# Kernel tuning notes

Hardware: AMD Instinct MI355X
Metric: run time of the kernel (lower is better)

## Reference

```python
import jax, jax.numpy as jnp
import numpy as np

B, S, D = 2, 2048, 1024
H, HD = 16, 64          # num_heads, head_dim
K = 32                  # JL n_components


def setup_inputs() -> dict:
    key = jax.random.key(0)
    k1, k2, k3, k4 = jax.random.split(key, 4)
    return {
        "hidden_states": jax.random.normal(k1, (B, S, D), dtype=jnp.float32),
        "W_attn": jax.random.normal(k2, (D, 3 * D), dtype=jnp.float32) * 0.02,
        "b_attn": jnp.zeros((3 * D,), dtype=jnp.float32),
        "S_proj": jax.random.normal(k3, (K, HD), dtype=jnp.float32) / np.sqrt(K),
        "W_proj": jax.random.normal(k4, (D, D), dtype=jnp.float32) * 0.02,
        "b_proj": jnp.zeros((D,), dtype=jnp.float32),
    }


def reference(hidden_states, W_attn, b_attn, S_proj, W_proj, b_proj):
    b, s, d = hidden_states.shape
    # GPT2 Conv1D: x @ W + b, then split into q,k,v
    qkv = hidden_states @ W_attn + b_attn            # [B,S,3D]
    q, k, v = jnp.split(qkv, 3, axis=-1)
    # split heads -> [B,H,S,HD]
    def split_heads(x):
        return x.reshape(b, s, H, HD).transpose(0, 2, 1, 3)
    q = split_heads(q) @ S_proj.T                    # [B,H,S,K] JL-reduced
    k = split_heads(k) @ S_proj.T                    # [B,H,S,K]
    v = split_heads(v)                               # [B,H,S,HD]
    # naive attention: scale by sqrt(value head_dim) per GPT2 _attn
    scores = jnp.einsum("bhqk,bhsk->bhqs", q, k) / jnp.sqrt(
        jnp.asarray(HD, dtype=v.dtype))              # [B,H,S,S]
    causal = jnp.tril(jnp.ones((s, s), dtype=bool))
    mask_value = jnp.finfo(scores.dtype).min
    scores = jnp.where(causal, scores, mask_value)
    attn = jax.nn.softmax(scores, axis=-1)
    out = jnp.einsum("bhqs,bhsd->bhqd", attn, v)     # [B,H,S,HD]
    out = out.transpose(0, 2, 1, 3).reshape(b, s, d)  # merge heads
    return out @ W_proj + b_proj
```

## Files before the change

kernel.cpp:

```cpp
#include <hip/hip_runtime.h>
#include <hip/hip_bf16.h>
#include <stdint.h>

#define B_ 2
#define S_ 2048
#define D_ 1024
#define H_ 16
#define HD_ 64
#define KJL 32
#define N3 3072
#define N2 2048

typedef __attribute__((ext_vector_type(8))) __bf16 bf16x8;
typedef __attribute__((ext_vector_type(4))) float floatx4;
typedef __attribute__((ext_vector_type(4))) short short4v;
typedef __attribute__((ext_vector_type(2))) unsigned int uint2v;

__device__ __forceinline__ unsigned short f2b(float x) {
  union { float f; unsigned u; } v; v.f = x;
  unsigned r = v.u + 0x7fffu + ((v.u >> 16) & 1u);
  return (unsigned short)(r >> 16);
}

__device__ __forceinline__ unsigned int pkbf(float lo, float hi) {
  union { float f; unsigned u; } a, b;
  a.f = lo; b.f = hi;
  return __builtin_amdgcn_perm(b.u + 0x8000u, a.u + 0x8000u, 0x07060302u);
}

__device__ __forceinline__ void async16(const void* g, void* l) {
  __builtin_amdgcn_global_load_lds((__attribute__((address_space(1))) void*)(g),
                                   (__attribute__((address_space(3))) void*)(l),
                                   16, 0, 0);
}

__global__ __launch_bounds__(256)
void prep_kernel(const float* __restrict__ hidden, unsigned short* __restrict__ hB,
                 const float* __restrict__ W_attn, const float* __restrict__ b_attn,
                 const float* __restrict__ Sp, const float* __restrict__ W_proj,
                 unsigned short* __restrict__ Bt2, unsigned short* __restrict__ WpT,
                 float* __restrict__ bias2) {
  __shared__ float shmem[2048];
  const int bid = blockIdx.x;
  const int tid = threadIdx.x;

  if (bid < 512) {
    const int n4 = (B_ * S_ * D_) / 4;
    int i = bid * 256 + tid;
    for (; i < n4; i += 512 * 256) {
      float4 v = *(const float4*)(hidden + 4 * (size_t)i);
      short4v o = {(short)f2b(v.x), (short)f2b(v.y), (short)f2b(v.z), (short)f2b(v.w)};
      *(short4v*)(hB + 4 * (size_t)i) = o;
    }
  } else if (bid < 2560) {
    const float* in;
    unsigned short* out;
    int Cs, local;
    if (bid < 1536) { local = bid - 512;  in = W_attn + 2048; out = Bt2 + 1024 * 1024; Cs = N3; }
    else            { local = bid - 1536; in = W_proj;        out = WpT;               Cs = D_; }
    float (*t)[33] = (float(*)[33])shmem;
    int c0 = (local & 31) * 32, r0 = (local >> 5) * 32;
    int tx = tid & 31, ty = tid >> 5;
    for (int j = 0; j < 32; j += 8)
      t[ty + j][tx] = in[(size_t)(r0 + ty + j) * Cs + c0 + tx];
    __syncthreads();
    for (int j = 0; j < 32; j += 8)
      out[(size_t)(c0 + ty + j) * D_ + r0 + tx] = f2b(t[tx][ty + j]);
  } else {
    const int lb = bid - 2560;
    const int part = lb >> 6;
    const int h = (lb >> 2) & 15;
    const int dc = lb & 3;
    for (int i = tid; i < 32 * 64; i += 256) shmem[i] = Sp[i];
    __syncthreads();
    const float scale = part ? 1.0f : 0.125f * 1.44269504f;
    const int d = dc * 256 + tid;
    float w[64];
    const float* src = W_attn + (size_t)d * N3 + part * D_ + h * 64;
    for (int j = 0; j < 16; ++j) {
      float4 v = *(const float4*)&src[j * 4];
      w[j * 4 + 0] = v.x; w[j * 4 + 1] = v.y; w[j * 4 + 2] = v.z; w[j * 4 + 3] = v.w;
    }
    const int nbase = part * 512 + h * 32;
    for (int kjl = 0; kjl < 32; ++kjl) {
      float acc = 0.f;
      for (int hd = 0; hd < 64; ++hd) acc += w[hd] * shmem[kjl * 64 + hd];
      Bt2[(size_t)(nbase + kjl) * D_ + d] = f2b(acc * scale);
    }
    if (dc == 0 && tid < 32) {
      float acc = 0.f;
      for (int hd = 0; hd < 64; ++hd) acc += b_attn[part * D_ + h * 64 + hd] * shmem[tid * 64 + hd];
      bias2[nbase + tid] = acc * scale;
    }
  }
}

__global__ __launch_bounds__(256, 2)
void qkv2_gemm_kernel(const unsigned short* __restrict__ A,
                      const unsigned short* __restrict__ Bt,
                      const float* __restrict__ b_attn,
                      const float* __restrict__ bias2,
                      unsigned short* __restrict__ Qjl,
                      unsigned short* __restrict__ Kjl,
                      unsigned short* __restrict__ Vc) {
  __shared__ __align__(16) unsigned short As[2][128 * 32];
  __shared__ __align__(16) unsigned short Bs[2][128 * 32];
  const int tid = threadIdx.x;
  const int lane = tid & 63, wv = tid >> 6;
  const int quad = lane >> 4, col = lane & 15;
  const int wm = wv >> 1, wn = wv & 1;
  const int m0 = blockIdx.y * 128, n0 = blockIdx.x * 128;

  floatx4 acc[4][4] = {};

  for (int kk = 0; kk < D_; kk += 64) {
    for (int it = 0; it < 4; ++it) {
      int c = it * 256 + tid;
      int ks = c >> 9, row = (c >> 2) & 127, kc = c & 3;
      async16(A + (size_t)(m0 + row) * D_ + kk + ks * 32 + kc * 8,
              (unsigned short*)As + c * 8);
    }
    for (int it = 0; it < 4; ++it) {
      int c = it * 256 + tid;
      int ks = c >> 9, row = (c >> 2) & 127, kc = c & 3;
      async16(Bt + (size_t)(n0 + row) * D_ + kk + ks * 32 + kc * 8,
              (unsigned short*)Bs + c * 8);
    }
    asm volatile("s_waitcnt vmcnt(0)" ::: "memory");
    __syncthreads();
    for (int ks = 0; ks < 2; ++ks) {
      bf16x8 af[4], bfr[4];
      for (int mt = 0; mt < 4; ++mt)
        af[mt] = *(const bf16x8*)&As[ks][(wm * 64 + mt * 16 + col) * 32 + quad * 8];
      for (int nt = 0; nt < 4; ++nt)
        bfr[nt] = *(const bf16x8*)&Bs[ks][(wn * 64 + nt * 16 + col) * 32 + quad * 8];
      for (int mt = 0; mt < 4; ++mt)
        for (int nt = 0; nt < 4; ++nt)
          acc[mt][nt] = __builtin_amdgcn_mfma_f32_16x16x32_bf16(
              af[mt], bfr[nt], acc[mt][nt], 0, 0, 0);
    }
    __syncthreads();
  }

  const int pq = n0 >> 9;
  for (int mt = 0; mt < 4; ++mt) {
    int gm0 = m0 + wm * 64 + mt * 16 + quad * 4;
    int b = gm0 >> 11, s = gm0 & (S_ - 1);
    for (int nt = 0; nt < 4; ++nt) {
      int gn = n0 + wn * 64 + nt * 16 + col;
      if (pq >= 2) {
        int vcol = gn - 1024;
        float bs = b_attn[2048 + vcol];
        int h = vcol >> 6, hd = vcol & 63;
        short4v vv;
        for (int i = 0; i < 4; ++i)
          vv[i] = (short)f2b(acc[mt][nt][i] + bs);
        size_t idx = ((((size_t)(b * H_ + h) * 64 + (s >> 5)) * 64 + hd) * 32 + (s & 31));
        *(short4v*)&Vc[idx] = vv;
      } else {
        float bs = bias2[gn];
        int gl = gn & 511;
        int h = gl >> 5, kjl = gl & 31;
        unsigned short* dst = pq ? Kjl : Qjl;
        size_t base = ((size_t)(b * H_ + h) * S_ + s) * KJL + kjl;
        for (int i = 0; i < 4; ++i)
          dst[base + (size_t)i * KJL] = f2b(acc[mt][nt][i] + bs);
      }
    }
  }
}

__global__ __launch_bounds__(256, 2)
void attn_kernel(const unsigned short* __restrict__ Qjl,
                 const unsigned short* __restrict__ Kjl,
                 const unsigned short* __restrict__ Vc,
                 unsigned short* __restrict__ AO) {
  __shared__ __align__(16) unsigned short Ps[4][32 * 136];
  const int tid = threadIdx.x;
  const int lane = tid & 63, wv = tid >> 6;
  const int quad = lane >> 4, l15 = lane & 15;

  const int blk = blockIdx.x;
  const int bh = blk & 31;
  const int u = blk >> 5;
  const int a = u & 7;
  const int g = (u & 8) ? (15 - a) : a;
  const int rp = (u >> 4) & 1;
  const int pairid = wv >> 1;
  const int half = wv & 1;
  const int t = g * 4 + rp * 2 + pairid;
  const int b = bh >> 4, h = bh & 15;

  unsigned short* Pw = &Ps[wv][0];
  const int nch = g + 1;
  const int kb = half ? ((nch + 1) >> 1) : 0;
  const int ke = half ? nch : ((nch + 1) >> 1);
  const int lastc = nch - 1;
  const int r = t & 3;

  const int laneK = l15 * KJL + quad * 8;
  const int laneV = l15 * 32 + quad * 8;
  const unsigned short* Kp = Kjl + (size_t)bh * S_ * KJL + laneK + (size_t)kb * 128 * KJL;
  const unsigned short* Vp = Vc + (size_t)bh * (64 * 64 * 32) + laneV + (size_t)kb * 8192;

  bf16x8 aq[2];
  for (int qn = 0; qn < 2; ++qn)
    aq[qn] = *(const bf16x8*)&Qjl[(size_t)(bh * S_ + t * 32 + qn * 16 + l15) * KJL + quad * 8];

  floatx4 o[4][2] = {};
  floatx4 psum[2] = {};
  const floatx4 zz = {0.f, 0.f, 0.f, 0.f};

  for (int kt = kb; kt < ke; ++kt) {
    bf16x8 ak[8];
    for (int sm = 0; sm < 8; ++sm)
      ak[sm] = *(const bf16x8*)&Kp[sm * (16 * KJL)];
    bf16x8 bv[4][4];
    for (int ks = 0; ks < 4; ++ks)
      for (int md = 0; md < 4; ++md)
        bv[ks][md] = *(const bf16x8*)&Vp[ks * 2048 + md * 512];
    Kp += 128 * KJL;
    Vp += 8192;

    floatx4 sc[8][2];
    for (int sm = 0; sm < 8; ++sm)
      for (int qn = 0; qn < 2; ++qn)
        sc[sm][qn] = __builtin_amdgcn_mfma_f32_16x16x32_bf16(ak[sm], aq[qn], zz, 0, 0, 0);

    if (kt == lastc) {
      for (int qn = 0; qn < 2; ++qn) {
        int qloc = r * 32 + qn * 16 + l15;
        for (int sm = 0; sm < 8; ++sm)
          for (int i = 0; i < 4; ++i)
            if (sm * 16 + quad * 4 + i > qloc) sc[sm][qn][i] = -1e30f;
      }
    }

    for (int qn = 0; qn < 2; ++qn) {
      for (int sm = 0; sm < 8; ++sm) {
        float p0 = __builtin_amdgcn_exp2f(sc[sm][qn][0]);
        float p1 = __builtin_amdgcn_exp2f(sc[sm][qn][1]);
        float p2 = __builtin_amdgcn_exp2f(sc[sm][qn][2]);
        float p3 = __builtin_amdgcn_exp2f(sc[sm][qn][3]);
        psum[qn][0] += p0; psum[qn][1] += p1;
        psum[qn][2] += p2; psum[qn][3] += p3;
        uint2v pk2 = {pkbf(p0, p1), pkbf(p2, p3)};
        *(uint2v*)&Pw[(qn * 16 + l15) * 136 + sm * 16 + quad * 4] = pk2;
      }
    }

    for (int ks = 0; ks < 4; ++ks) {
      bf16x8 bp[2];
      for (int qn = 0; qn < 2; ++qn)
        bp[qn] = *(const bf16x8*)&Pw[(qn * 16 + l15) * 136 + ks * 32 + quad * 8];
      for (int qn = 0; qn < 2; ++qn)
        for (int md = 0; md < 4; ++md)
          o[md][qn] = __builtin_amdgcn_mfma_f32_16x16x32_bf16(bv[ks][md], bp[qn], o[md][qn], 0, 0, 0);
    }
  }

  float l0 = psum[0][0] + psum[0][1] + psum[0][2] + psum[0][3];
  float l1 = psum[1][0] + psum[1][1] + psum[1][2] + psum[1][3];
  l0 += __shfl_xor(l0, 16, 64); l0 += __shfl_xor(l0, 32, 64);
  l1 += __shfl_xor(l1, 16, 64); l1 += __shfl_xor(l1, 32, 64);

  if (half) {
    float* fp = (float*)Pw;
    for (int qn = 0; qn < 2; ++qn)
      for (int md = 0; md < 4; ++md)
        *(floatx4*)(fp + (qn * 4 + md) * 256 + lane * 4) = o[md][qn];
    fp[2048 + lane] = l0;
    fp[2112 + lane] = l1;
  }
  __syncthreads();

  if (!half) {
    const float* fq = (const float*)(&Ps[wv | 1][0]);
    float inv0 = 1.f / (l0 + fq[2048 + lane]);
    float inv1 = 1.f / (l1 + fq[2112 + lane]);
    for (int qn = 0; qn < 2; ++qn) {
      float inv = qn ? inv1 : inv0;
      for (int md = 0; md < 4; ++md) {
        floatx4 p = *(const floatx4*)(fq + (qn * 4 + md) * 256 + lane * 4);
        floatx4 s = o[md][qn];
        uint2v t4 = {pkbf((s[0] + p[0]) * inv, (s[1] + p[1]) * inv),
                     pkbf((s[2] + p[2]) * inv, (s[3] + p[3]) * inv)};
        *(uint2v*)&Pw[(qn * 16 + l15) * 72 + md * 16 + quad * 4] = t4;
      }
    }
    asm volatile("s_waitcnt lgkmcnt(0)" ::: "memory");
    int q = lane >> 1, hf = lane & 1;
    size_t gbase = ((size_t)(b * S_ + t * 32 + q)) * D_ + h * HD_ + hf * 32;
    for (int jj = 0; jj < 4; ++jj) {
      bf16x8 v = *(const bf16x8*)&Pw[q * 72 + hf * 32 + jj * 8];
      *(bf16x8*)&AO[gbase + jj * 8] = v;
    }
  }
}

__global__ __launch_bounds__(256, 2)
void proj_gemm_kernel(const unsigned short* __restrict__ A,
                      const unsigned short* __restrict__ Bt,
                      const float* __restrict__ bias,
                      float* __restrict__ out) {
  __shared__ __align__(16) unsigned short As[2][64 * 32];
  __shared__ __align__(16) unsigned short Bs[2][128 * 32];
  const int tid = threadIdx.x;
  const int lane = tid & 63, wv = tid >> 6;
  const int quad = lane >> 4, col = lane & 15;
  const int wm = wv >> 1, wn = wv & 1;
  const int m0 = blockIdx.y * 64, n0 = blockIdx.x * 128;

  floatx4 acc[2][4] = {};

  for (int kk = 0; kk < D_; kk += 64) {
    for (int it = 0; it < 2; ++it) {
      int c = it * 256 + tid;
      int ks = c >> 8, row = (c >> 2) & 63, kc = c & 3;
      async16(A + (size_t)(m0 + row) * D_ + kk + ks * 32 + kc * 8,
              (unsigned short*)As + c * 8);
    }
    for (int it = 0; it < 4; ++it) {
      int c = it * 256 + tid;
      int ks = c >> 9, row = (c >> 2) & 127, kc = c & 3;
      async16(Bt + (size_t)(n0 + row) * D_ + kk + ks * 32 + kc * 8,
              (unsigned short*)Bs + c * 8);
    }
    asm volatile("s_waitcnt vmcnt(0)" ::: "memory");
    __syncthreads();
    for (int ks = 0; ks < 2; ++ks) {
      bf16x8 af[2], bfr[4];
      for (int mt = 0; mt < 2; ++mt)
        af[mt] = *(const bf16x8*)&As[ks][(wm * 32 + mt * 16 + col) * 32 + quad * 8];
      for (int nt = 0; nt < 4; ++nt)
        bfr[nt] = *(const bf16x8*)&Bs[ks][(wn * 64 + nt * 16 + col) * 32 + quad * 8];
      for (int mt = 0; mt < 2; ++mt)
        for (int nt = 0; nt < 4; ++nt)
          acc[mt][nt] = __builtin_amdgcn_mfma_f32_16x16x32_bf16(
              af[mt], bfr[nt], acc[mt][nt], 0, 0, 0);
    }
    __syncthreads();
  }

  for (int mt = 0; mt < 2; ++mt) {
    int gm0 = m0 + wm * 32 + mt * 16 + quad * 4;
    for (int nt = 0; nt < 4; ++nt) {
      int gn = n0 + wn * 64 + nt * 16 + col;
      float bs = bias[gn];
      for (int i = 0; i < 4; ++i)
        out[(size_t)(gm0 + i) * D_ + gn] = acc[mt][nt][i] + bs;
    }
  }
}

extern "C" void kernel_launch(void* const* d_in, const int* in_sizes, int n_in,
                              void* d_out, int out_size, void* d_ws, size_t ws_size,
                              hipStream_t stream) {
  (void)in_sizes; (void)n_in; (void)out_size; (void)ws_size;
  const float* hidden = (const float*)d_in[0];
  const float* W_attn = (const float*)d_in[1];
  const float* b_attn = (const float*)d_in[2];
  const float* S_proj = (const float*)d_in[3];
  const float* W_proj = (const float*)d_in[4];
  const float* b_proj = (const float*)d_in[5];
  float* out = (float*)d_out;

  char* ws = (char*)d_ws;
  unsigned short* hB    = (unsigned short*)(ws);
  unsigned short* Bt2   = (unsigned short*)(ws + (8u << 20));
  unsigned short* WpT   = (unsigned short*)(ws + (12u << 20));
  float*          bias2 = (float*)         (ws + (14u << 20));
  unsigned short* Qjl   = (unsigned short*)(ws + (15u << 20));
  unsigned short* Kjl   = (unsigned short*)(ws + (19u << 20));
  unsigned short* Vc    = (unsigned short*)(ws + (23u << 20));
  unsigned short* AO    = (unsigned short*)(ws + (31u << 20));

  prep_kernel<<<2688, 256, 0, stream>>>(hidden, hB, W_attn, b_attn, S_proj,
                                        W_proj, Bt2, WpT, bias2);
  qkv2_gemm_kernel<<<dim3(N2 / 128, (B_ * S_) / 128), 256, 0, stream>>>(
      hB, Bt2, b_attn, bias2, Qjl, Kjl, Vc);
  attn_kernel<<<1024, 256, 0, stream>>>(Qjl, Kjl, Vc, AO);
  proj_gemm_kernel<<<dim3(D_ / 128, (B_ * S_) / 64), 256, 0, stream>>>(
      AO, WpT, b_proj, out);
}
```

Measured before the change: 183.2 us.

## Double-buffer K loads across chunks, pair query tiles, and raise MFMA priority

Each wave pair now takes query tile u or its mirror 63-u, so causal work is balanced inside a block instead of across blocks. The K-tile loop is unrolled by two with ping-pong register buffers, so the next chunk's K fragments are fetched while the current chunk's softmax and PV MFMAs run. MFMA sections are wrapped in s_setprio to favour matrix issue. This raises register pressure and could cut occupancy at launch bounds (256,2), and the two waves in a block may now have unequal chunk counts.

```diff
diff --git a/kernel.cpp b/kernel.cpp
--- a/kernel.cpp
+++ b/kernel.cpp
@@ -183,16 +183,13 @@
   const int blk = blockIdx.x;
   const int bh = blk & 31;
   const int u = blk >> 5;
-  const int a = u & 7;
-  const int g = (u & 8) ? (15 - a) : a;
-  const int rp = (u >> 4) & 1;
   const int pairid = wv >> 1;
   const int half = wv & 1;
-  const int t = g * 4 + rp * 2 + pairid;
+  const int t = pairid ? (63 - u) : u;
   const int b = bh >> 4, h = bh & 15;
 
   unsigned short* Pw = &Ps[wv][0];
-  const int nch = g + 1;
+  const int nch = (t >> 2) + 1;
   const int kb = half ? ((nch + 1) >> 1) : 0;
   const int ke = half ? nch : ((nch + 1) >> 1);
   const int lastc = nch - 1;
@@ -211,53 +208,73 @@
   floatx4 psum[2] = {};
   const floatx4 zz = {0.f, 0.f, 0.f, 0.f};
 
-  for (int kt = kb; kt < ke; ++kt) {
-    bf16x8 ak[8];
-    for (int sm = 0; sm < 8; ++sm)
-      ak[sm] = *(const bf16x8*)&Kp[sm * (16 * KJL)];
-    bf16x8 bv[4][4];
-    for (int ks = 0; ks < 4; ++ks)
-      for (int md = 0; md < 4; ++md)
-        bv[ks][md] = *(const bf16x8*)&Vp[ks * 2048 + md * 512];
-    Kp += 128 * KJL;
-    Vp += 8192;
-
-    floatx4 sc[8][2];
-    for (int sm = 0; sm < 8; ++sm)
-      for (int qn = 0; qn < 2; ++qn)
-        sc[sm][qn] = __builtin_amdgcn_mfma_f32_16x16x32_bf16(ak[sm], aq[qn], zz, 0, 0, 0);
-
-    if (kt == lastc) {
-      for (int qn = 0; qn < 2; ++qn) {
-        int qloc = r * 32 + qn * 16 + l15;
-        for (int sm = 0; sm < 8; ++sm)
-          for (int i = 0; i < 4; ++i)
-            if (sm * 16 + quad * 4 + i > qloc) sc[sm][qn][i] = -1e30f;
-      }
-    }
-
-    for (int qn = 0; qn < 2; ++qn) {
-      for (int sm = 0; sm < 8; ++sm) {
-        float p0 = __builtin_amdgcn_exp2f(sc[sm][qn][0]);
-        float p1 = __builtin_amdgcn_exp2f(sc[sm][qn][1]);
-        float p2 = __builtin_amdgcn_exp2f(sc[sm][qn][2]);
-        float p3 = __builtin_amdgcn_exp2f(sc[sm][qn][3]);
-        psum[qn][0] += p0; psum[qn][1] += p1;
-        psum[qn][2] += p2; psum[qn][3] += p3;
-        uint2v pk2 = {pkbf(p0, p1), pkbf(p2, p3)};
-        *(uint2v*)&Pw[(qn * 16 + l15) * 136 + sm * 16 + quad * 4] = pk2;
-      }
-    }
-
-    for (int ks = 0; ks < 4; ++ks) {
-      bf16x8 bp[2];
-      for (int qn = 0; qn < 2; ++qn)
-        bp[qn] = *(const bf16x8*)&Pw[(qn * 16 + l15) * 136 + ks * 32 + quad * 8];
-      for (int qn = 0; qn < 2; ++qn)
-        for (int md = 0; md < 4; ++md)
-          o[md][qn] = __builtin_amdgcn_mfma_f32_16x16x32_bf16(bv[ks][md], bp[qn], o[md][qn], 0, 0, 0);
-    }
-  }
+  bf16x8 akA[8], akB[8];
+
+#define LOADK_(dst)                                                         \
+  {                                                                         \
+    _Pragma("unroll") for (int sm = 0; sm < 8; ++sm)                        \
+        dst[sm] = *(const bf16x8*)&Kp[sm * (16 * KJL)];                     \
+    Kp += 128 * KJL;                                                        \
+  }
+
+#define CHUNK_(akc, akn, dopf, kt_)                                         \
+  {                                                                         \
+    bf16x8 bv[4][4];                                                        \
+    _Pragma("unroll") for (int ks = 0; ks < 4; ++ks)                        \
+      _Pragma("unroll") for (int md = 0; md < 4; ++md)                      \
+          bv[ks][md] = *(const bf16x8*)&Vp[ks * 2048 + md * 512];           \
+    Vp += 8192;                                                             \
+    floatx4 sc[8][2];                                                       \
+    __builtin_amdgcn_s_setprio(1);                                          \
+    _Pragma("unroll") for (int sm = 0; sm < 8; ++sm)                        \
+      _Pragma("unroll") for (int qn = 0; qn < 2; ++qn)                      \
+          sc[sm][qn] = __builtin_amdgcn_mfma_f32_16x16x32_bf16(             \
+              akc[sm], aq[qn], zz, 0, 0, 0);                                \
+    __builtin_amdgcn_s_setprio(0);                                          \
+    if (dopf) LOADK_(akn);                                                  \
+    if ((kt_) == lastc) {                                                   \
+      _Pragma("unroll") for (int qn = 0; qn < 2; ++qn) {                    \
+        int qloc = r * 32 + qn * 16 + l15;                                  \
+        _Pragma("unroll") for (int sm = 0; sm < 8; ++sm)                    \
+          _Pragma("unroll") for (int i = 0; i < 4; ++i)                     \
+              if (sm * 16 + quad * 4 + i > qloc) sc[sm][qn][i] = -1e30f;    \
+      }                                                                     \
+    }                                                                       \
+    _Pragma("unroll") for (int qn = 0; qn < 2; ++qn) {                      \
+      _Pragma("unroll") for (int sm = 0; sm < 8; ++sm) {                    \
+        floatx4 pe;                                                         \
+        pe[0] = __builtin_amdgcn_exp2f(sc[sm][qn][0]);                      \
+        pe[1] = __builtin_amdgcn_exp2f(sc[sm][qn][1]);                      \
+        pe[2] = __builtin_amdgcn_exp2f(sc[sm][qn][2]);                      \
+        pe[3] = __builtin_amdgcn_exp2f(sc[sm][qn][3]);                      \
+        psum[qn] += pe;                                                     \
+        uint2v pk2 = {pkbf(pe[0], pe[1]), pkbf(pe[2], pe[3])};              \
+        *(uint2v*)&Pw[(qn * 16 + l15) * 136 + sm * 16 + quad * 4] = pk2;    \
+      }                                                                     \
+    }                                                                       \
+    _Pragma("unroll") for (int ks = 0; ks < 4; ++ks) {                      \
+      bf16x8 bp[2];                                                         \
+      _Pragma("unroll") for (int qn = 0; qn < 2; ++qn)                      \
+          bp[qn] = *(const bf16x8*)&Pw[(qn * 16 + l15) * 136 + ks * 32 + quad * 8]; \
+      __builtin_amdgcn_s_setprio(1);                                        \
+      _Pragma("unroll") for (int qn = 0; qn < 2; ++qn)                      \
+        _Pragma("unroll") for (int md = 0; md < 4; ++md)                    \
+            o[md][qn] = __builtin_amdgcn_mfma_f32_16x16x32_bf16(            \
+                bv[ks][md], bp[qn], o[md][qn], 0, 0, 0);                    \
+      __builtin_amdgcn_s_setprio(0);                                        \
+    }                                                                       \
+  }
+
+  int kt = kb;
+  if (kt < ke) LOADK_(akA);
+  for (; kt + 2 <= ke; kt += 2) {
+    CHUNK_(akA, akB, 1, kt);
+    CHUNK_(akB, akA, (kt + 2 < ke), kt + 1);
+  }
+  if (kt < ke) CHUNK_(akA, akB, 0, kt);
+
+#undef LOADK_
+#undef CHUNK_
 
   float l0 = psum[0][0] + psum[0][1] + psum[0][2] + psum[0][3];
   float l1 = psum[1][0] + psum[1][1] + psum[1][2] + psum[1][3];
```

Measured after the change: 218.7 us. 1.19x slower.

## Split each query tile's key range across four waves and raise MFMA priority

Applied to the files above, without the earlier changes.

Each block now handles one 32-row query tile, with its causal key chunks split across all four waves instead of two pairs of waves each covering half. The grid doubles to 2048 blocks, and wave 0 reduces the partial outputs and row sums from the other three waves through shared memory. This targets load imbalance from the causal triangle and the long serial key loop per wave, at the cost of more blocks and a heavier reduction step. s_setprio is raised around the MFMA sequences to favour matrix-issuing waves.

```diff
diff --git a/kernel.cpp b/kernel.cpp
--- a/kernel.cpp
+++ b/kernel.cpp
@@ -182,19 +182,13 @@
 
   const int blk = blockIdx.x;
   const int bh = blk & 31;
-  const int u = blk >> 5;
-  const int a = u & 7;
-  const int g = (u & 8) ? (15 - a) : a;
-  const int rp = (u >> 4) & 1;
-  const int pairid = wv >> 1;
-  const int half = wv & 1;
-  const int t = g * 4 + rp * 2 + pairid;
+  const int t = blk >> 5;
   const int b = bh >> 4, h = bh & 15;
 
   unsigned short* Pw = &Ps[wv][0];
-  const int nch = g + 1;
-  const int kb = half ? ((nch + 1) >> 1) : 0;
-  const int ke = half ? nch : ((nch + 1) >> 1);
+  const int nch = (t >> 2) + 1;
+  const int kb = (wv * nch) >> 2;
+  const int ke = ((wv + 1) * nch) >> 2;
   const int lastc = nch - 1;
   const int r = t & 3;
 
@@ -223,9 +217,11 @@
     Vp += 8192;
 
     floatx4 sc[8][2];
+    __builtin_amdgcn_s_setprio(1);
     for (int sm = 0; sm < 8; ++sm)
       for (int qn = 0; qn < 2; ++qn)
         sc[sm][qn] = __builtin_amdgcn_mfma_f32_16x16x32_bf16(ak[sm], aq[qn], zz, 0, 0, 0);
+    __builtin_amdgcn_s_setprio(0);
 
     if (kt == lastc) {
       for (int qn = 0; qn < 2; ++qn) {
@@ -253,9 +249,11 @@
       bf16x8 bp[2];
       for (int qn = 0; qn < 2; ++qn)
         bp[qn] = *(const bf16x8*)&Pw[(qn * 16 + l15) * 136 + ks * 32 + quad * 8];
+      __builtin_amdgcn_s_setprio(1);
       for (int qn = 0; qn < 2; ++qn)
         for (int md = 0; md < 4; ++md)
           o[md][qn] = __builtin_amdgcn_mfma_f32_16x16x32_bf16(bv[ks][md], bp[qn], o[md][qn], 0, 0, 0);
+      __builtin_amdgcn_s_setprio(0);
     }
   }
 
@@ -264,7 +262,7 @@
   l0 += __shfl_xor(l0, 16, 64); l0 += __shfl_xor(l0, 32, 64);
   l1 += __shfl_xor(l1, 16, 64); l1 += __shfl_xor(l1, 32, 64);
 
-  if (half) {
+  if (wv) {
     float* fp = (float*)Pw;
     for (int qn = 0; qn < 2; ++qn)
       for (int md = 0; md < 4; ++md)
@@ -274,17 +272,23 @@
   }
   __syncthreads();
 
-  if (!half) {
-    const float* fq = (const float*)(&Ps[wv | 1][0]);
-    float inv0 = 1.f / (l0 + fq[2048 + lane]);
-    float inv1 = 1.f / (l1 + fq[2112 + lane]);
+  if (!wv) {
+    for (int p = 1; p < 4; ++p) {
+      const float* fq = (const float*)(&Ps[p][0]);
+      l0 += fq[2048 + lane];
+      l1 += fq[2112 + lane];
+      for (int qn = 0; qn < 2; ++qn)
+        for (int md = 0; md < 4; ++md)
+          o[md][qn] += *(const floatx4*)(fq + (qn * 4 + md) * 256 + lane * 4);
+    }
+    float inv0 = 1.f / l0;
+    float inv1 = 1.f / l1;
     for (int qn = 0; qn < 2; ++qn) {
       float inv = qn ? inv1 : inv0;
       for (int md = 0; md < 4; ++md) {
-        floatx4 p = *(const floatx4*)(fq + (qn * 4 + md) * 256 + lane * 4);
         floatx4 s = o[md][qn];
-        uint2v t4 = {pkbf((s[0] + p[0]) * inv, (s[1] + p[1]) * inv),
-                     pkbf((s[2] + p[2]) * inv, (s[3] + p[3]) * inv)};
+        uint2v t4 = {pkbf(s[0] * inv, s[1] * inv),
+                     pkbf(s[2] * inv, s[3] * inv)};
         *(uint2v*)&Pw[(qn * 16 + l15) * 72 + md * 16 + quad * 4] = t4;
       }
     }
@@ -379,7 +383,7 @@
                                         W_proj, Bt2, WpT, bias2);
   qkv2_gemm_kernel<<<dim3(N2 / 128, (B_ * S_) / 128), 256, 0, stream>>>(
       hB, Bt2, b_attn, bias2, Qjl, Kjl, Vc);
-  attn_kernel<<<1024, 256, 0, stream>>>(Qjl, Kjl, Vc, AO);
+  attn_kernel<<<2048, 256, 0, stream>>>(Qjl, Kjl, Vc, AO);
   proj_gemm_kernel<<<dim3(D_ / 128, (B_ * S_) / 64), 256, 0, stream>>>(
       AO, WpT, b_proj, out);
 }
```

New measurement: 181.5 us. No clear change (-0.9%).
